# Kernel tuning notes

Measured on AMD Instinct MI355X. Metric: run time of the kernel, lower is better.

## Reference

```python
import jax, jax.numpy as jnp
import numpy as np

B, D, C = 4096, 1024, 11003
SCALE = 28.0
EPS_LS = 0.1
T = 4.0
L2, L3, L4 = 1.0, 1.0, 1.0
ALPHA, BETA = 0.6, 0.4
SPOS, SNEG = 10.0, 40.0
HDR_ALPHA, HDR_BETA, PLEN = 3.0, 3.0, 63


def setup_inputs() -> dict:
    key = jax.random.key(0)
    k1, k2, k3, k4, k5 = jax.random.split(key, 5)
    return {
        "visual_embed": jax.random.normal(k1, (B, D), dtype=jnp.float32),
        "textual_embed": jax.random.normal(k2, (B, D), dtype=jnp.float32),
        "labels": jax.random.randint(k3, (B,), 0, C, dtype=jnp.int64)
        if jax.config.read("jax_enable_x64") else jax.random.randint(k3, (B,), 0, C, dtype=jnp.int32),
        "W": jax.random.normal(k4, (D, C), dtype=jnp.float32) * (6.0 / (D + C)) ** 0.5,
        "W_text": jax.random.normal(k5, (D, C), dtype=jnp.float32) * (6.0 / (D + C)) ** 0.5,
    }


def _l2norm(x, axis):
    return x / jnp.linalg.norm(x, axis=axis, keepdims=True)


def _label_smooth_ce(logits, labels):
    # CrossEntropyLabelSmooth with epsilon=0.1
    lp = jax.nn.log_softmax(logits, axis=1)
    n, c = logits.shape
    picked = jnp.take_along_axis(lp, labels[:, None], axis=1)[:, 0]
    return -((1.0 - EPS_LS) * picked + (EPS_LS / c) * lp.sum(axis=1)).mean()


def _pdist(e, eps=1e-12):
    sq = (e * e).sum(axis=1)
    d2 = jnp.maximum(sq[:, None] + sq[None, :] - 2.0 * (e @ e.T), eps)
    d = jnp.sqrt(d2)
    return d * (1.0 - jnp.eye(e.shape[0], dtype=d.dtype))  # zero diagonal


def _hard_dark_rank(student, teacher):
    score_t = -HDR_ALPHA * _pdist(teacher) ** HDR_BETA
    score_s = -HDR_ALPHA * _pdist(student) ** HDR_BETA
    # top PLEN neighbors of teacher (skip self at rank 0), descending sort
    permute_idx = jnp.argsort(-score_t, axis=1)[:, 1 : PLEN + 1]  # [B, PLEN]
    ordered = jnp.take_along_axis(score_s, permute_idx, axis=1)  # [B, PLEN]
    # logsumexp over suffixes ordered[:, i:] == reversed cumulative logsumexp
    rev = jnp.flip(ordered, axis=1)
    lse_tail = jnp.flip(jax.lax.cumlogsumexp(rev, axis=1), axis=1)
    log_prob = (ordered - lse_tail).sum(axis=1)
    return (-log_prob).mean()


def _kl_div(student_logits, teacher_logits):
    s = jax.nn.softmax(student_logits / T, axis=1)
    t = jax.nn.softmax(jax.lax.stop_gradient(teacher_logits) / T, axis=1)
    log_s = jnp.log(jnp.maximum(s, 1e-12))
    log_t = jnp.log(jnp.maximum(t, 1e-12))
    return (((log_t - log_s) * t).sum(axis=1)).mean()


def reference(visual_embed, textual_embed, labels, W, W_text):
    vn = _l2norm(visual_embed, axis=1)
    tn = _l2norm(textual_embed, axis=1)
    Wn = W / jnp.linalg.norm(W, axis=0, keepdims=True)
    Wtn = W_text / jnp.linalg.norm(W_text, axis=0, keepdims=True)

    visual_logits = SCALE * (vn @ Wn)   # [B, C]
    textual_logits = SCALE * (tn @ Wn)  # [B, C]

    v_loss = _label_smooth_ce(visual_logits, labels)
    t_loss = _label_smooth_ce(textual_logits, labels)

    # distillation (LAMBDA2 feature L2 + LAMBDA3 KL on logits)
    vf = jax.lax.stop_gradient(vn)
    dist_f = ((vf - tn) ** 2).sum(axis=1).mean()
    dist_p = _kl_div(textual_logits, visual_logits)
    distillation = L2 * dist_f + L3 * dist_p

    # W_text filter CE (LAMBDA4 branch)
    t_filter = L4 * _label_smooth_ce(SCALE * (tn @ Wtn), labels)

    # HardDarkRank (Flickr30K branch): student=textual, teacher=detached visual
    loss_hdr = _hard_dark_rank(tn, jax.lax.stop_gradient(vn))

    instance = v_loss + t_loss + t_filter + distillation + 0.1 * loss_hdr

    # global_align_loss, fully vectorized. The original loops over rows AND
    # columns so every (i,j) pair is counted twice.
    sim = vn @ tn.T  # [B, B]
    mask = labels[:, None] == labels[None, :]
    loss_pos = jnp.log1p(jnp.exp(-SPOS * (sim - ALPHA)))
    loss_neg = jnp.log1p(jnp.exp(SNEG * (sim - BETA)))
    global_align = 2.0 * jnp.where(mask, loss_pos, loss_neg).sum() / sim.shape[0]

    return instance + global_align
```

## Files before the change

kernel.cpp:

```cpp
#include <hip/hip_runtime.h>
#include <math.h>

#define Bn 4096
#define Dn 1024
#define Cn 11003
#define Cpad 11008
#define NCTL 86
#define NQ 9
#define NT 32
#define NTRI 528

typedef __attribute__((ext_vector_type(8))) short bf16x8;
typedef __attribute__((ext_vector_type(4))) float f32x4;

__device__ __forceinline__ unsigned short f2bf(float f) {
  union { float f; unsigned u; } v; v.f = f;
  unsigned r = (v.u + 0x7fffu + ((v.u >> 16) & 1u)) >> 16;
  return (unsigned short)r;
}
__device__ __forceinline__ float bf2f(unsigned short h) {
  union { unsigned u; float f; } v; v.u = ((unsigned)h) << 16;
  return v.f;
}

__device__ __forceinline__ void stage16(const unsigned short* g, unsigned short* l) {
  __builtin_amdgcn_global_load_lds(
      (const __attribute__((address_space(1))) void*)g,
      (__attribute__((address_space(3))) void*)l, 16, 0, 0);
}

#define SRC_BLK(tid) (((tid) & 7) ^ (((tid) >> 3) & 7))
#define FRAG(buf, R, KB) (*(const bf16x8*)((buf) + (R) * 64 + (((KB) ^ ((R) & 7)) * 8)))

__device__ __forceinline__ float blk_sum256(float v, volatile float* sb) {
#pragma unroll
  for (int o = 32; o > 0; o >>= 1) v += __shfl_down(v, o, 64);
  __syncthreads();
  if ((threadIdx.x & 63) == 0) sb[threadIdx.x >> 6] = v;
  __syncthreads();
  return sb[0] + sb[1] + sb[2] + sb[3];
}

__global__ void zero_acc_k(float* acc) {
  if (threadIdx.x < 8) acc[threadIdx.x] = 0.f;
}

__global__ __launch_bounds__(256) void rownorm_k(const float* __restrict__ x,
                                                 unsigned short* __restrict__ yh,
                                                 float* __restrict__ sq) {
  __shared__ float sb[4];
  int r = blockIdx.x;
  const float* xr = x + (size_t)r * Dn;
  float s = 0.f;
  for (int k = threadIdx.x; k < Dn; k += 256) { float v = xr[k]; s += v * v; }
  s = blk_sum256(s, sb);
  float nrm = sqrtf(s);
  float s2 = 0.f;
  for (int k = threadIdx.x; k < Dn; k += 256) {
    float v = xr[k] / nrm;
    yh[(size_t)r * Dn + k] = f2bf(v);
    s2 += v * v;
  }
  s2 = blk_sum256(s2, sb);
  if (threadIdx.x == 0) sq[r] = s2;
}

__global__ __launch_bounds__(256) void colnorm_k(const float* __restrict__ W,
                                                 float* __restrict__ rn) {
  int c = blockIdx.x * 256 + threadIdx.x;
  if (c >= Cn) return;
  float s = 0.f;
  for (int d = 0; d < Dn; ++d) { float v = W[(size_t)d * Cn + c]; s += v * v; }
  rn[c] = 1.f / sqrtf(s);
}

__global__ __launch_bounds__(256) void transpose_k(const float* __restrict__ W,
                                                   const float* __restrict__ rn,
                                                   unsigned short* __restrict__ WT) {
  __shared__ float T[64][65];
  const int c0 = blockIdx.x * 64, d0 = blockIdx.y * 64;
  const int tid = threadIdx.x;
  const int cl = tid & 63;
  for (int dl = tid >> 6; dl < 64; dl += 4) {
    float v = (c0 + cl < Cn) ? W[(size_t)(d0 + dl) * Cn + c0 + cl] : 0.f;
    T[cl][dl] = v;
  }
  __syncthreads();
  const int dd = tid & 63;
  for (int co = tid >> 6; co < 64; co += 4) {
    int c = c0 + co;
    unsigned short o = 0;
    if (c < Cn) o = f2bf(T[co][dd] * rn[c]);
    WT[(size_t)c * Dn + d0 + dd] = o;
  }
}

__global__ __launch_bounds__(256, 2) void logits_vt_k(
    const unsigned short* __restrict__ vnh, const unsigned short* __restrict__ tnh,
    const unsigned short* __restrict__ WnT, float* __restrict__ part) {
  __shared__ __align__(16) unsigned short Av[128 * 64];
  __shared__ __align__(16) unsigned short At[128 * 64];
  __shared__ __align__(16) unsigned short Bs[128 * 64];
  __shared__ float qsum[7 * 128];

  const int rt = blockIdx.x, ct = blockIdx.y;
  const int r0 = rt * 128, c0 = ct * 128;
  const int tid = threadIdx.x;
  const int lane = tid & 63;
  const int wid = tid >> 6;
  const int wr = (wid >> 1) * 64, wc = (wid & 1) * 64;
  const int m = lane & 15, q = lane >> 4;

  for (int t = tid; t < 7 * 128; t += 256) qsum[t] = 0.f;

  const f32x4 zero4 = {0.f, 0.f, 0.f, 0.f};
  f32x4 accV[4][4], accT[4][4];
#pragma unroll
  for (int i = 0; i < 4; ++i)
#pragma unroll
    for (int j = 0; j < 4; ++j) { accV[i][j] = zero4; accT[i][j] = zero4; }

  const int srow = tid >> 3;
  const int skc = SRC_BLK(tid) * 8;

  for (int kk = 0; kk < 16; ++kk) {
    const int k0 = kk * 64;
#pragma unroll
    for (int p = 0; p < 4; ++p) {
      stage16(vnh + (size_t)(r0 + p * 32 + srow) * Dn + k0 + skc, Av + p * 2048 + tid * 8);
      stage16(tnh + (size_t)(r0 + p * 32 + srow) * Dn + k0 + skc, At + p * 2048 + tid * 8);
      stage16(WnT + (size_t)(c0 + p * 32 + srow) * Dn + k0 + skc, Bs + p * 2048 + tid * 8);
    }
    __syncthreads();
#pragma unroll
    for (int ks = 0; ks < 2; ++ks) {
      const int KB = ks * 4 + q;
      bf16x8 av[4], at[4], bb[4];
#pragma unroll
      for (int f = 0; f < 4; ++f) {
        av[f] = FRAG(Av, wr + f * 16 + m, KB);
        at[f] = FRAG(At, wr + f * 16 + m, KB);
        bb[f] = FRAG(Bs, wc + f * 16 + m, KB);
      }
#pragma unroll
      for (int i = 0; i < 4; ++i)
#pragma unroll
        for (int j = 0; j < 4; ++j) {
          accV[i][j] = __builtin_amdgcn_mfma_f32_16x16x32_bf16(av[i], bb[j], accV[i][j], 0, 0, 0);
          accT[i][j] = __builtin_amdgcn_mfma_f32_16x16x32_bf16(at[i], bb[j], accT[i][j], 0, 0, 0);
        }
    }
    __syncthreads();
  }

#pragma unroll
  for (int i = 0; i < 4; ++i) {
#pragma unroll
    for (int r = 0; r < 4; ++r) {
      const int rowl = wr + i * 16 + q * 4 + r;
      float s0 = 0.f, s1 = 0.f, s2 = 0.f, s3 = 0.f, s6 = 0.f, s7 = 0.f, s8 = 0.f;
#pragma unroll
      for (int j = 0; j < 4; ++j) {
        int col = c0 + wc + j * 16 + m;
        if (col < Cn) {
          float V = 28.f * accV[i][j][r];
          float T = 28.f * accT[i][j][r];
          float ev4 = __expf((V - 28.f) * 0.25f);
          float et4 = __expf((T - 28.f) * 0.25f);
          float ev2 = ev4 * ev4, et2 = et4 * et4;
          s0 += ev2 * ev2;
          s1 += V;
          s2 += et2 * et2;
          s3 += T;
          s6 += ev4;
          s7 += et4;
          s8 += ev4 * (V - T);
        }
      }
#pragma unroll
      for (int o = 1; o < 16; o <<= 1) {
        s0 += __shfl_xor(s0, o, 64); s1 += __shfl_xor(s1, o, 64);
        s2 += __shfl_xor(s2, o, 64); s3 += __shfl_xor(s3, o, 64);
        s6 += __shfl_xor(s6, o, 64); s7 += __shfl_xor(s7, o, 64);
        s8 += __shfl_xor(s8, o, 64);
      }
      if (m == 0) {
        atomicAdd(&qsum[0 * 128 + rowl], s0);
        atomicAdd(&qsum[1 * 128 + rowl], s1);
        atomicAdd(&qsum[2 * 128 + rowl], s2);
        atomicAdd(&qsum[3 * 128 + rowl], s3);
        atomicAdd(&qsum[4 * 128 + rowl], s6);
        atomicAdd(&qsum[5 * 128 + rowl], s7);
        atomicAdd(&qsum[6 * 128 + rowl], s8);
      }
    }
  }
  __syncthreads();
  if (tid < 128) {
    size_t base = (size_t)ct * Bn + r0 + tid;
    const size_t qs = (size_t)NCTL * Bn;
    part[0 * qs + base] = qsum[0 * 128 + tid];
    part[1 * qs + base] = qsum[1 * 128 + tid];
    part[2 * qs + base] = qsum[2 * 128 + tid];
    part[3 * qs + base] = qsum[3 * 128 + tid];
    part[6 * qs + base] = qsum[4 * 128 + tid];
    part[7 * qs + base] = qsum[5 * 128 + tid];
    part[8 * qs + base] = qsum[6 * 128 + tid];
  }
}

__global__ __launch_bounds__(256, 2) void logits_f_k(
    const unsigned short* __restrict__ tnh, const unsigned short* __restrict__ WtnT,
    float* __restrict__ part) {
  __shared__ __align__(16) unsigned short Aa[256 * 64];
  __shared__ __align__(16) unsigned short Bs[128 * 64];
  __shared__ float qsum[2 * 256];

  const int rt = blockIdx.x, ct = blockIdx.y;
  const int r0 = rt * 256, c0 = ct * 128;
  const int tid = threadIdx.x;
  const int lane = tid & 63;
  const int wid = tid >> 6;
  const int wr = (wid >> 1) * 128, wc = (wid & 1) * 64;
  const int m = lane & 15, q = lane >> 4;

  for (int t = tid; t < 2 * 256; t += 256) qsum[t] = 0.f;

  const f32x4 zero4 = {0.f, 0.f, 0.f, 0.f};
  f32x4 acc[8][4];
#pragma unroll
  for (int i = 0; i < 8; ++i)
#pragma unroll
    for (int j = 0; j < 4; ++j) acc[i][j] = zero4;

  const int srow = tid >> 3;
  const int skc = SRC_BLK(tid) * 8;

  for (int kk = 0; kk < 16; ++kk) {
    const int k0 = kk * 64;
#pragma unroll
    for (int p = 0; p < 8; ++p)
      stage16(tnh + (size_t)(r0 + p * 32 + srow) * Dn + k0 + skc, Aa + p * 2048 + tid * 8);
#pragma unroll
    for (int p = 0; p < 4; ++p)
      stage16(WtnT + (size_t)(c0 + p * 32 + srow) * Dn + k0 + skc, Bs + p * 2048 + tid * 8);
    __syncthreads();
#pragma unroll
    for (int ks = 0; ks < 2; ++ks) {
      const int KB = ks * 4 + q;
      bf16x8 aa[8], bb[4];
#pragma unroll
      for (int f = 0; f < 8; ++f) aa[f] = FRAG(Aa, wr + f * 16 + m, KB);
#pragma unroll
      for (int f = 0; f < 4; ++f) bb[f] = FRAG(Bs, wc + f * 16 + m, KB);
#pragma unroll
      for (int i = 0; i < 8; ++i)
#pragma unroll
        for (int j = 0; j < 4; ++j)
          acc[i][j] = __builtin_amdgcn_mfma_f32_16x16x32_bf16(aa[i], bb[j], acc[i][j], 0, 0, 0);
    }
    __syncthreads();
  }

#pragma unroll
  for (int i = 0; i < 8; ++i) {
#pragma unroll
    for (int r = 0; r < 4; ++r) {
      const int rowl = wr + i * 16 + q * 4 + r;
      float s4 = 0.f, s5 = 0.f;
#pragma unroll
      for (int j = 0; j < 4; ++j) {
        int col = c0 + wc + j * 16 + m;
        if (col < Cn) {
          float F = 28.f * acc[i][j][r];
          s4 += __expf(F - 28.f);
          s5 += F;
        }
      }
#pragma unroll
      for (int o = 1; o < 16; o <<= 1) {
        s4 += __shfl_xor(s4, o, 64);
        s5 += __shfl_xor(s5, o, 64);
      }
      if (m == 0) {
        atomicAdd(&qsum[0 * 256 + rowl], s4);
        atomicAdd(&qsum[1 * 256 + rowl], s5);
      }
    }
  }
  __syncthreads();
  {
    size_t base = (size_t)ct * Bn + r0 + tid;
    const size_t qs = (size_t)NCTL * Bn;
    part[4 * qs + base] = qsum[0 * 256 + tid];
    part[5 * qs + base] = qsum[1 * 256 + tid];
  }
}

__global__ __launch_bounds__(256, 3) void gramsym_f32_k(const unsigned short* __restrict__ A,
                                                        float* __restrict__ G) {
  __shared__ __align__(16) unsigned short Aa[128 * 64];
  __shared__ __align__(16) unsigned short Bs[128 * 64];
  int t = blockIdx.x, it = 0, rem = NT;
  while (t >= rem) { t -= rem; ++it; --rem; }
  const int jt = it + t;
  const int i0 = it * 128, j0 = jt * 128;
  const int tid = threadIdx.x;
  const int lane = tid & 63;
  const int wid = tid >> 6;
  const int wr = (wid >> 1) * 64, wc = (wid & 1) * 64;
  const int m = lane & 15, q = lane >> 4;

  const f32x4 zero4 = {0.f, 0.f, 0.f, 0.f};
  f32x4 acc[4][4];
#pragma unroll
  for (int i = 0; i < 4; ++i)
#pragma unroll
    for (int j = 0; j < 4; ++j) acc[i][j] = zero4;

  const int srow = tid >> 3;
  const int skc = SRC_BLK(tid) * 8;

  for (int kk = 0; kk < 16; ++kk) {
    const int k0 = kk * 64;
#pragma unroll
    for (int p = 0; p < 4; ++p) {
      stage16(A + (size_t)(i0 + p * 32 + srow) * Dn + k0 + skc, Aa + p * 2048 + tid * 8);
      stage16(A + (size_t)(j0 + p * 32 + srow) * Dn + k0 + skc, Bs + p * 2048 + tid * 8);
    }
    __syncthreads();
#pragma unroll
    for (int ks = 0; ks < 2; ++ks) {
      const int KB = ks * 4 + q;
      bf16x8 aa[4], bb[4];
#pragma unroll
      for (int f = 0; f < 4; ++f) {
        aa[f] = FRAG(Aa, wr + f * 16 + m, KB);
        bb[f] = FRAG(Bs, wc + f * 16 + m, KB);
      }
#pragma unroll
      for (int i = 0; i < 4; ++i)
#pragma unroll
        for (int j = 0; j < 4; ++j)
          acc[i][j] = __builtin_amdgcn_mfma_f32_16x16x32_bf16(aa[i], bb[j], acc[i][j], 0, 0, 0);
    }
    __syncthreads();
  }
#pragma unroll
  for (int i = 0; i < 4; ++i)
#pragma unroll
    for (int j = 0; j < 4; ++j)
#pragma unroll
      for (int r = 0; r < 4; ++r) {
        int row = wr + i * 16 + q * 4 + r, col = wc + j * 16 + m;
        G[(size_t)(i0 + row) * Bn + j0 + col] = acc[i][j][r];
        if (it != jt) G[(size_t)(j0 + col) * Bn + i0 + row] = acc[i][j][r];
      }
}

__global__ __launch_bounds__(256, 3) void gramsym_bf16_k(const unsigned short* __restrict__ A,
                                                         unsigned short* __restrict__ G) {
  __shared__ __align__(16) unsigned short Aa[128 * 64];
  __shared__ __align__(16) unsigned short Bs[128 * 64];
  int t = blockIdx.x, it = 0, rem = NT;
  while (t >= rem) { t -= rem; ++it; --rem; }
  const int jt = it + t;
  const int i0 = it * 128, j0 = jt * 128;
  const int tid = threadIdx.x;
  const int lane = tid & 63;
  const int wid = tid >> 6;
  const int wr = (wid >> 1) * 64, wc = (wid & 1) * 64;
  const int m = lane & 15, q = lane >> 4;

  const f32x4 zero4 = {0.f, 0.f, 0.f, 0.f};
  f32x4 acc[4][4];
#pragma unroll
  for (int i = 0; i < 4; ++i)
#pragma unroll
    for (int j = 0; j < 4; ++j) acc[i][j] = zero4;

  const int srow = tid >> 3;
  const int skc = SRC_BLK(tid) * 8;

  for (int kk = 0; kk < 16; ++kk) {
    const int k0 = kk * 64;
#pragma unroll
    for (int p = 0; p < 4; ++p) {
      stage16(A + (size_t)(i0 + p * 32 + srow) * Dn + k0 + skc, Aa + p * 2048 + tid * 8);
      stage16(A + (size_t)(j0 + p * 32 + srow) * Dn + k0 + skc, Bs + p * 2048 + tid * 8);
    }
    __syncthreads();
#pragma unroll
    for (int ks = 0; ks < 2; ++ks) {
      const int KB = ks * 4 + q;
      bf16x8 aa[4], bb[4];
#pragma unroll
      for (int f = 0; f < 4; ++f) {
        aa[f] = FRAG(Aa, wr + f * 16 + m, KB);
        bb[f] = FRAG(Bs, wc + f * 16 + m, KB);
      }
#pragma unroll
      for (int i = 0; i < 4; ++i)
#pragma unroll
        for (int j = 0; j < 4; ++j)
          acc[i][j] = __builtin_amdgcn_mfma_f32_16x16x32_bf16(aa[i], bb[j], acc[i][j], 0, 0, 0);
    }
    __syncthreads();
  }
#pragma unroll
  for (int i = 0; i < 4; ++i)
#pragma unroll
    for (int j = 0; j < 4; ++j)
#pragma unroll
      for (int r = 0; r < 4; ++r) {
        int row = wr + i * 16 + q * 4 + r, col = wc + j * 16 + m;
        unsigned short h = f2bf(acc[i][j][r]);
        G[(size_t)(i0 + row) * Bn + j0 + col] = h;
        if (it != jt) G[(size_t)(j0 + col) * Bn + i0 + row] = h;
      }
}

__global__ __launch_bounds__(256, 3) void align_k(const unsigned short* __restrict__ vnh,
                                                  const unsigned short* __restrict__ tnh,
                                                  const int* __restrict__ labels,
                                                  float* __restrict__ accbuf) {
  __shared__ __align__(16) unsigned short Aa[128 * 64];
  __shared__ __align__(16) unsigned short Bs[128 * 64];
  __shared__ int li_s[128], lj_s[128];
  __shared__ float sb[4];
  const int jt = blockIdx.x, it = blockIdx.y;
  const int j0 = jt * 128, i0 = it * 128;
  const int tid = threadIdx.x;
  const int lane = tid & 63;
  const int wid = tid >> 6;
  const int wr = (wid >> 1) * 64, wc = (wid & 1) * 64;
  const int m = lane & 15, q = lane >> 4;

  if (tid < 128) li_s[tid] = labels[i0 + tid];
  else lj_s[tid - 128] = labels[j0 + tid - 128];

  const f32x4 zero4 = {0.f, 0.f, 0.f, 0.f};
  f32x4 acc[4][4];
#pragma unroll
  for (int i = 0; i < 4; ++i)
#pragma unroll
    for (int j = 0; j < 4; ++j) acc[i][j] = zero4;

  const int srow = tid >> 3;
  const int skc = SRC_BLK(tid) * 8;

  for (int kk = 0; kk < 16; ++kk) {
    const int k0 = kk * 64;
#pragma unroll
    for (int p = 0; p < 4; ++p) {
      stage16(vnh + (size_t)(i0 + p * 32 + srow) * Dn + k0 + skc, Aa + p * 2048 + tid * 8);
      stage16(tnh + (size_t)(j0 + p * 32 + srow) * Dn + k0 + skc, Bs + p * 2048 + tid * 8);
    }
    __syncthreads();
#pragma unroll
    for (int ks = 0; ks < 2; ++ks) {
      const int KB = ks * 4 + q;
      bf16x8 aa[4], bb[4];
#pragma unroll
      for (int f = 0; f < 4; ++f) {
        aa[f] = FRAG(Aa, wr + f * 16 + m, KB);
        bb[f] = FRAG(Bs, wc + f * 16 + m, KB);
      }
#pragma unroll
      for (int i = 0; i < 4; ++i)
#pragma unroll
        for (int j = 0; j < 4; ++j)
          acc[i][j] = __builtin_amdgcn_mfma_f32_16x16x32_bf16(aa[i], bb[j], acc[i][j], 0, 0, 0);
    }
    __syncthreads();
  }

  float ls = 0.f;
#pragma unroll
  for (int i = 0; i < 4; ++i)
#pragma unroll
    for (int r = 0; r < 4; ++r) {
      int li = li_s[wr + i * 16 + q * 4 + r];
#pragma unroll
      for (int j = 0; j < 4; ++j) {
        int lj = lj_s[wc + j * 16 + m];
        float s = acc[i][j][r];
        float x = (li == lj) ? (-10.f * (s - 0.6f)) : (40.f * (s - 0.4f));
        ls += fmaxf(x, 0.f) + __logf(1.f + __expf(-fabsf(x)));
      }
    }
  float tot = blk_sum256(ls, sb);
  if (tid == 0) atomicAdd(&accbuf[1], tot);
}

__global__ __launch_bounds__(256) void picked_k(const unsigned short* __restrict__ vnh,
                                                const unsigned short* __restrict__ tnh,
                                                const unsigned short* __restrict__ WnT,
                                                const unsigned short* __restrict__ WtnT,
                                                const int* __restrict__ labels,
                                                float* __restrict__ pv, float* __restrict__ pt,
                                                float* __restrict__ pf, float* __restrict__ df) {
  __shared__ float sb[4];
  int r = blockIdx.x;
  int lab = labels[r];
  float spv = 0.f, spt = 0.f, spf = 0.f, sdf = 0.f;
  for (int k = threadIdx.x; k < Dn; k += 256) {
    float a = bf2f(vnh[(size_t)r * Dn + k]);
    float b = bf2f(tnh[(size_t)r * Dn + k]);
    float w = bf2f(WnT[(size_t)lab * Dn + k]);
    float wt = bf2f(WtnT[(size_t)lab * Dn + k]);
    spv += a * w;
    spt += b * w;
    spf += b * wt;
    float dd = a - b;
    sdf += dd * dd;
  }
  spv = blk_sum256(spv, sb);
  spt = blk_sum256(spt, sb);
  spf = blk_sum256(spf, sb);
  sdf = blk_sum256(sdf, sb);
  if (threadIdx.x == 0) {
    pv[r] = 28.f * spv;
    pt[r] = 28.f * spt;
    pf[r] = 28.f * spf;
    df[r] = sdf;
  }
}

__global__ __launch_bounds__(256) void finalize_k(const float* __restrict__ part,
                                                  const float* __restrict__ pv,
                                                  const float* __restrict__ pt,
                                                  const float* __restrict__ pf,
                                                  const float* __restrict__ df,
                                                  float* __restrict__ accbuf) {
  __shared__ float sb[4];
  int r = blockIdx.x * 256 + threadIdx.x;
  float s[NQ];
#pragma unroll
  for (int q = 0; q < NQ; ++q) s[q] = 0.f;
  const size_t qs = (size_t)NCTL * Bn;
  for (int ct = 0; ct < NCTL; ++ct) {
#pragma unroll
    for (int q = 0; q < NQ; ++q) s[q] += part[(size_t)q * qs + (size_t)ct * Bn + r];
  }
  float lseV = logf(s[0]) + 28.f;
  float lseT = logf(s[2]) + 28.f;
  float lseF = logf(s[4]) + 28.f;
  const float invC = 1.f / (float)Cn;
  float ceV = -(0.9f * (pv[r] - lseV) + 0.1f * invC * (s[1] - (float)Cn * lseV));
  float ceT = -(0.9f * (pt[r] - lseT) + 0.1f * invC * (s[3] - (float)Cn * lseT));
  float ceF = -(0.9f * (pf[r] - lseF) + 0.1f * invC * (s[5] - (float)Cn * lseF));
  float kl = s[8] / (4.f * s[6]) + logf(s[7]) - logf(s[6]);
  float row = ceV + ceT + ceF + kl + df[r];
  float tot = blk_sum256(row, sb);
  if (threadIdx.x == 0) atomicAdd(&accbuf[0], tot / (float)Bn);
}

__device__ __forceinline__ int kswz(int j) {
  return (j & ~63) | ((j ^ (j >> 6)) & 63);
}
__device__ __forceinline__ unsigned long long shflx_u64(unsigned long long v, int o) {
  int lo = __shfl_xor((int)(unsigned)v, o, 64);
  int hi = __shfl_xor((int)(unsigned)(v >> 32), o, 64);
  return ((unsigned long long)(unsigned)hi << 32) | (unsigned)lo;
}

__global__ __launch_bounds__(256) void hdr_k(const float* __restrict__ Gv,
                                             const unsigned short* __restrict__ Gtb,
                                             const float* __restrict__ sqv,
                                             const float* __restrict__ sqt,
                                             float* __restrict__ accbuf) {
  __shared__ float key[Bn];
  __shared__ int selIdx[64];
  __shared__ float selS[64];
  const int i = blockIdx.x, tid = threadIdx.x;
  const int lane = tid & 63, wid = tid >> 6;
  const float INF = __builtin_inff();
  float sqi = sqv[i];
  const float4* gv4 = (const float4*)(Gv + (size_t)i * Bn);
  const float4* sq4 = (const float4*)sqv;
  for (int j4 = tid; j4 < Bn / 4; j4 += 256) {
    float4 g = gv4[j4];
    float4 s = sq4[j4];
    int j = j4 * 4;
    key[kswz(j + 0)] = (j + 0 == i) ? INF : fmaxf(sqi + s.x - 2.f * g.x, 1e-12f);
    key[kswz(j + 1)] = (j + 1 == i) ? INF : fmaxf(sqi + s.y - 2.f * g.y, 1e-12f);
    key[kswz(j + 2)] = (j + 2 == i) ? INF : fmaxf(sqi + s.z - 2.f * g.z, 1e-12f);
    key[kswz(j + 3)] = (j + 3 == i) ? INF : fmaxf(sqi + s.w - 2.f * g.w, 1e-12f);
  }
  __syncthreads();

  if (wid == 0) {
    unsigned long long best = ~0ull;
    for (int k = 0; k < 64; ++k) {
      int j = k * 64 + lane;
      float v = key[kswz(j)];
      unsigned long long p = ((unsigned long long)__float_as_uint(v) << 32) | (unsigned)j;
      if (p < best) best = p;
    }
    for (int it = 0; it < 63; ++it) {
      unsigned long long w = best;
#pragma unroll
      for (int o = 32; o > 0; o >>= 1) {
        unsigned long long ow = shflx_u64(w, o);
        if (ow < w) w = ow;
      }
      int bj = (int)(unsigned)w;
      if (lane == 0) selIdx[it] = bj;
      int s = bj & 63;
      int kj = (lane << 6) | s;
      int sidx = kswz(kj);
      float kv = key[sidx];
      if (kj == bj) { kv = INF; key[sidx] = INF; }
      unsigned long long p = ((unsigned long long)__float_as_uint(kv) << 32) | (unsigned)kj;
#pragma unroll
      for (int o = 32; o > 0; o >>= 1) {
        unsigned long long op = shflx_u64(p, o);
        if (op < p) p = op;
      }
      if (lane == s) best = p;
    }
  }
  __syncthreads();

  if (tid < 63) {
    int j = selIdx[tid];
    float g = bf2f(Gtb[(size_t)i * Bn + j]);
    float d2 = fmaxf(sqt[i] + sqt[j] - 2.f * g, 1e-12f);
    selS[tid] = -3.f * sqrtf(d2) * d2;
  }
  __syncthreads();

  if (tid == 0) {
    float lse = selS[62];
    float loss = 0.f;
    for (int k = 61; k >= 0; --k) {
      float a = fmaxf(lse, selS[k]);
      lse = a + logf(__expf(lse - a) + __expf(selS[k] - a));
      loss += lse - selS[k];
    }
    atomicAdd(&accbuf[2], loss);
  }
}

__global__ void combine_k(const float* __restrict__ accbuf, float* __restrict__ out) {
  out[0] = accbuf[0] + (2.f / (float)Bn) * accbuf[1] + (0.1f / (float)Bn) * accbuf[2];
}

extern "C" void kernel_launch(void* const* d_in, const int* in_sizes, int n_in,
                              void* d_out, int out_size, void* d_ws, size_t ws_size,
                              hipStream_t stream) {
  const float* ve = (const float*)d_in[0];
  const float* te = (const float*)d_in[1];
  const int* labels = (const int*)d_in[2];
  const float* W = (const float*)d_in[3];
  const float* Wt = (const float*)d_in[4];
  float* out = (float*)d_out;

  char* base = (char*)d_ws;
  size_t off = 0;
  unsigned short* vnh = (unsigned short*)(base + off);  off += (size_t)Bn * Dn * 2;
  unsigned short* tnh = (unsigned short*)(base + off);  off += (size_t)Bn * Dn * 2;
  unsigned short* WnT = (unsigned short*)(base + off);  off += (size_t)Cpad * Dn * 2;
  unsigned short* WtnT = (unsigned short*)(base + off); off += (size_t)Cpad * Dn * 2;
  float* Gv = (float*)(base + off);          off += (size_t)Bn * Bn * 4;
  unsigned short* Gtb = (unsigned short*)(base + off); off += (size_t)Bn * Bn * 2;
  float* part = (float*)(base + off);        off += (size_t)NQ * NCTL * Bn * 4;
  float* rnW = (float*)(base + off);         off += (size_t)Cpad * 4;
  float* rnWt = (float*)(base + off);        off += (size_t)Cpad * 4;
  float* sqv = (float*)(base + off);         off += (size_t)Bn * 4;
  float* sqt = (float*)(base + off);         off += (size_t)Bn * 4;
  float* pv = (float*)(base + off);          off += (size_t)Bn * 4;
  float* pt = (float*)(base + off);          off += (size_t)Bn * 4;
  float* pf = (float*)(base + off);          off += (size_t)Bn * 4;
  float* df = (float*)(base + off);          off += (size_t)Bn * 4;
  float* acc = (float*)(base + off);         off += 64;

  zero_acc_k<<<1, 64, 0, stream>>>(acc);
  rownorm_k<<<Bn, 256, 0, stream>>>(ve, vnh, sqv);
  rownorm_k<<<Bn, 256, 0, stream>>>(te, tnh, sqt);
  colnorm_k<<<(Cn + 255) / 256, 256, 0, stream>>>(W, rnW);
  colnorm_k<<<(Cn + 255) / 256, 256, 0, stream>>>(Wt, rnWt);
  transpose_k<<<dim3(Cpad / 64, Dn / 64), 256, 0, stream>>>(W, rnW, WnT);
  transpose_k<<<dim3(Cpad / 64, Dn / 64), 256, 0, stream>>>(Wt, rnWt, WtnT);
  logits_vt_k<<<dim3(Bn / 128, NCTL), 256, 0, stream>>>(vnh, tnh, WnT, part);
  logits_f_k<<<dim3(Bn / 256, NCTL), 256, 0, stream>>>(tnh, WtnT, part);
  gramsym_f32_k<<<NTRI, 256, 0, stream>>>(vnh, Gv);
  gramsym_bf16_k<<<NTRI, 256, 0, stream>>>(tnh, Gtb);
  align_k<<<dim3(Bn / 128, Bn / 128), 256, 0, stream>>>(vnh, tnh, labels, acc);
  picked_k<<<Bn, 256, 0, stream>>>(vnh, tnh, WnT, WtnT, labels, pv, pt, pf, df);
  finalize_k<<<Bn / 256, 256, 0, stream>>>(part, pv, pt, pf, df, acc);
  hdr_k<<<Bn, 256, 0, stream>>>(Gv, Gtb, sqv, sqt, acc);
  combine_k<<<1, 1, 0, stream>>>(acc, out);
}
```

Baseline: 979.0 us.

## Switch logits GEMMs to 32x32 MFMA, fuse gram with align, merge launches

The logits kernels now use the 32x32x16 bf16 MFMA instruction instead of 16x16x32, which means fewer LDS fragment reads per FLOP, and the row reductions are reworked to match the new accumulator layout. The symmetric f32 visual gram kernel and the align kernel are fused into one full-grid kernel. It shares the visual A tile, computes both G and the align loss, and writes G without using symmetry. The paired norm, colnorm and transpose launches are each merged into a single launch through a grid dimension. The fused kernel gives up the triangular saving on the visual gram, trading extra MFMA work for one fewer pass over the inputs.

```diff
diff --git a/kernel.cpp b/kernel.cpp
--- a/kernel.cpp
+++ b/kernel.cpp
@@ -12,6 +12,7 @@
 
 typedef __attribute__((ext_vector_type(8))) short bf16x8;
 typedef __attribute__((ext_vector_type(4))) float f32x4;
+typedef __attribute__((ext_vector_type(16))) float f32x16;
 
 __device__ __forceinline__ unsigned short f2bf(float f) {
   union { float f; unsigned u; } v; v.f = f;
@@ -45,10 +46,16 @@
   if (threadIdx.x < 8) acc[threadIdx.x] = 0.f;
 }
 
-__global__ __launch_bounds__(256) void rownorm_k(const float* __restrict__ x,
-                                                 unsigned short* __restrict__ yh,
-                                                 float* __restrict__ sq) {
+__global__ __launch_bounds__(256) void rownorm_k(const float* __restrict__ xv,
+                                                 const float* __restrict__ xt,
+                                                 unsigned short* __restrict__ yv,
+                                                 unsigned short* __restrict__ yt,
+                                                 float* __restrict__ sqv,
+                                                 float* __restrict__ sqt) {
   __shared__ float sb[4];
+  const float* x = blockIdx.y ? xt : xv;
+  unsigned short* y = blockIdx.y ? yt : yv;
+  float* sq = blockIdx.y ? sqt : sqv;
   int r = blockIdx.x;
   const float* xr = x + (size_t)r * Dn;
   float s = 0.f;
@@ -58,7 +65,7 @@
   float s2 = 0.f;
   for (int k = threadIdx.x; k < Dn; k += 256) {
     float v = xr[k] / nrm;
-    yh[(size_t)r * Dn + k] = f2bf(v);
+    y[(size_t)r * Dn + k] = f2bf(v);
     s2 += v * v;
   }
   s2 = blk_sum256(s2, sb);
@@ -66,23 +73,33 @@
 }
 
 __global__ __launch_bounds__(256) void colnorm_k(const float* __restrict__ W,
-                                                 float* __restrict__ rn) {
+                                                 const float* __restrict__ Wt,
+                                                 float* __restrict__ rnW,
+                                                 float* __restrict__ rnWt) {
+  const float* X = blockIdx.y ? Wt : W;
+  float* rn = blockIdx.y ? rnWt : rnW;
   int c = blockIdx.x * 256 + threadIdx.x;
   if (c >= Cn) return;
   float s = 0.f;
-  for (int d = 0; d < Dn; ++d) { float v = W[(size_t)d * Cn + c]; s += v * v; }
+  for (int d = 0; d < Dn; ++d) { float v = X[(size_t)d * Cn + c]; s += v * v; }
   rn[c] = 1.f / sqrtf(s);
 }
 
 __global__ __launch_bounds__(256) void transpose_k(const float* __restrict__ W,
-                                                   const float* __restrict__ rn,
-                                                   unsigned short* __restrict__ WT) {
+                                                   const float* __restrict__ Wt,
+                                                   const float* __restrict__ rnW,
+                                                   const float* __restrict__ rnWt,
+                                                   unsigned short* __restrict__ WnT,
+                                                   unsigned short* __restrict__ WtnT) {
   __shared__ float T[64][65];
+  const float* X = blockIdx.z ? Wt : W;
+  const float* rn = blockIdx.z ? rnWt : rnW;
+  unsigned short* WT = blockIdx.z ? WtnT : WnT;
   const int c0 = blockIdx.x * 64, d0 = blockIdx.y * 64;
   const int tid = threadIdx.x;
   const int cl = tid & 63;
   for (int dl = tid >> 6; dl < 64; dl += 4) {
-    float v = (c0 + cl < Cn) ? W[(size_t)(d0 + dl) * Cn + c0 + cl] : 0.f;
+    float v = (c0 + cl < Cn) ? X[(size_t)(d0 + dl) * Cn + c0 + cl] : 0.f;
     T[cl][dl] = v;
   }
   __syncthreads();
@@ -109,16 +126,17 @@
   const int lane = tid & 63;
   const int wid = tid >> 6;
   const int wr = (wid >> 1) * 64, wc = (wid & 1) * 64;
-  const int m = lane & 15, q = lane >> 4;
+  const int l31 = lane & 31, half = lane >> 5;
 
   for (int t = tid; t < 7 * 128; t += 256) qsum[t] = 0.f;
 
-  const f32x4 zero4 = {0.f, 0.f, 0.f, 0.f};
-  f32x4 accV[4][4], accT[4][4];
-#pragma unroll
-  for (int i = 0; i < 4; ++i)
-#pragma unroll
-    for (int j = 0; j < 4; ++j) { accV[i][j] = zero4; accT[i][j] = zero4; }
+  f32x16 accV[2][2], accT[2][2];
+#pragma unroll
+  for (int i = 0; i < 2; ++i)
+#pragma unroll
+    for (int j = 0; j < 2; ++j)
+#pragma unroll
+      for (int e = 0; e < 16; ++e) { accV[i][j][e] = 0.f; accT[i][j][e] = 0.f; }
 
   const int srow = tid >> 3;
   const int skc = SRC_BLK(tid) * 8;
@@ -133,38 +151,38 @@
     }
     __syncthreads();
 #pragma unroll
-    for (int ks = 0; ks < 2; ++ks) {
-      const int KB = ks * 4 + q;
-      bf16x8 av[4], at[4], bb[4];
-#pragma unroll
-      for (int f = 0; f < 4; ++f) {
-        av[f] = FRAG(Av, wr + f * 16 + m, KB);
-        at[f] = FRAG(At, wr + f * 16 + m, KB);
-        bb[f] = FRAG(Bs, wc + f * 16 + m, KB);
-      }
-#pragma unroll
-      for (int i = 0; i < 4; ++i)
-#pragma unroll
-        for (int j = 0; j < 4; ++j) {
-          accV[i][j] = __builtin_amdgcn_mfma_f32_16x16x32_bf16(av[i], bb[j], accV[i][j], 0, 0, 0);
-          accT[i][j] = __builtin_amdgcn_mfma_f32_16x16x32_bf16(at[i], bb[j], accT[i][j], 0, 0, 0);
+    for (int t = 0; t < 4; ++t) {
+      const int KB = t * 2 + half;
+      bf16x8 av[2], at[2], bb[2];
+#pragma unroll
+      for (int f = 0; f < 2; ++f) {
+        av[f] = FRAG(Av, wr + f * 32 + l31, KB);
+        at[f] = FRAG(At, wr + f * 32 + l31, KB);
+        bb[f] = FRAG(Bs, wc + f * 32 + l31, KB);
+      }
+#pragma unroll
+      for (int i = 0; i < 2; ++i)
+#pragma unroll
+        for (int j = 0; j < 2; ++j) {
+          accV[i][j] = __builtin_amdgcn_mfma_f32_32x32x16_bf16(av[i], bb[j], accV[i][j], 0, 0, 0);
+          accT[i][j] = __builtin_amdgcn_mfma_f32_32x32x16_bf16(at[i], bb[j], accT[i][j], 0, 0, 0);
         }
     }
     __syncthreads();
   }
 
 #pragma unroll
-  for (int i = 0; i < 4; ++i) {
-#pragma unroll
-    for (int r = 0; r < 4; ++r) {
-      const int rowl = wr + i * 16 + q * 4 + r;
+  for (int bi = 0; bi < 2; ++bi) {
+#pragma unroll
+    for (int r = 0; r < 16; ++r) {
+      const int rowl = wr + bi * 32 + (r & 3) + 8 * (r >> 2) + 4 * half;
       float s0 = 0.f, s1 = 0.f, s2 = 0.f, s3 = 0.f, s6 = 0.f, s7 = 0.f, s8 = 0.f;
 #pragma unroll
-      for (int j = 0; j < 4; ++j) {
-        int col = c0 + wc + j * 16 + m;
+      for (int bj = 0; bj < 2; ++bj) {
+        int col = c0 + wc + bj * 32 + l31;
         if (col < Cn) {
-          float V = 28.f * accV[i][j][r];
-          float T = 28.f * accT[i][j][r];
+          float V = 28.f * accV[bi][bj][r];
+          float T = 28.f * accT[bi][bj][r];
           float ev4 = __expf((V - 28.f) * 0.25f);
           float et4 = __expf((T - 28.f) * 0.25f);
           float ev2 = ev4 * ev4, et2 = et4 * et4;
@@ -178,13 +196,13 @@
         }
       }
 #pragma unroll
-      for (int o = 1; o < 16; o <<= 1) {
+      for (int o = 1; o < 32; o <<= 1) {
         s0 += __shfl_xor(s0, o, 64); s1 += __shfl_xor(s1, o, 64);
         s2 += __shfl_xor(s2, o, 64); s3 += __shfl_xor(s3, o, 64);
         s6 += __shfl_xor(s6, o, 64); s7 += __shfl_xor(s7, o, 64);
         s8 += __shfl_xor(s8, o, 64);
       }
-      if (m == 0) {
+      if (l31 == 0) {
         atomicAdd(&qsum[0 * 128 + rowl], s0);
         atomicAdd(&qsum[1 * 128 + rowl], s1);
         atomicAdd(&qsum[2 * 128 + rowl], s2);
@@ -222,16 +240,17 @@
   const int lane = tid & 63;
   const int wid = tid >> 6;
   const int wr = (wid >> 1) * 128, wc = (wid & 1) * 64;
-  const int m = lane & 15, q = lane >> 4;
+  const int l31 = lane & 31, half = lane >> 5;
 
   for (int t = tid; t < 2 * 256; t += 256) qsum[t] = 0.f;
 
-  const f32x4 zero4 = {0.f, 0.f, 0.f, 0.f};
-  f32x4 acc[8][4];
-#pragma unroll
-  for (int i = 0; i < 8; ++i)
-#pragma unroll
-    for (int j = 0; j < 4; ++j) acc[i][j] = zero4;
+  f32x16 acc[4][2];
+#pragma unroll
+  for (int i = 0; i < 4; ++i)
+#pragma unroll
+    for (int j = 0; j < 2; ++j)
+#pragma unroll
+      for (int e = 0; e < 16; ++e) acc[i][j][e] = 0.f;
 
   const int srow = tid >> 3;
   const int skc = SRC_BLK(tid) * 8;
@@ -246,43 +265,43 @@
       stage16(WtnT + (size_t)(c0 + p * 32 + srow) * Dn + k0 + skc, Bs + p * 2048 + tid * 8);
     __syncthreads();
 #pragma unroll
-    for (int ks = 0; ks < 2; ++ks) {
-      const int KB = ks * 4 + q;
-      bf16x8 aa[8], bb[4];
-#pragma unroll
-      for (int f = 0; f < 8; ++f) aa[f] = FRAG(Aa, wr + f * 16 + m, KB);
-#pragma unroll
-      for (int f = 0; f < 4; ++f) bb[f] = FRAG(Bs, wc + f * 16 + m, KB);
-#pragma unroll
-      for (int i = 0; i < 8; ++i)
-#pragma unroll
-        for (int j = 0; j < 4; ++j)
-          acc[i][j] = __builtin_amdgcn_mfma_f32_16x16x32_bf16(aa[i], bb[j], acc[i][j], 0, 0, 0);
-    }
-    __syncthreads();
-  }
-
-#pragma unroll
-  for (int i = 0; i < 8; ++i) {
-#pragma unroll
-    for (int r = 0; r < 4; ++r) {
-      const int rowl = wr + i * 16 + q * 4 + r;
+    for (int t = 0; t < 4; ++t) {
+      const int KB = t * 2 + half;
+      bf16x8 aa[4], bb[2];
+#pragma unroll
+      for (int f = 0; f < 4; ++f) aa[f] = FRAG(Aa, wr + f * 32 + l31, KB);
+#pragma unroll
+      for (int f = 0; f < 2; ++f) bb[f] = FRAG(Bs, wc + f * 32 + l31, KB);
+#pragma unroll
+      for (int i = 0; i < 4; ++i)
+#pragma unroll
+        for (int j = 0; j < 2; ++j)
+          acc[i][j] = __builtin_amdgcn_mfma_f32_32x32x16_bf16(aa[i], bb[j], acc[i][j], 0, 0, 0);
+    }
+    __syncthreads();
+  }
+
+#pragma unroll
+  for (int bi = 0; bi < 4; ++bi) {
+#pragma unroll
+    for (int r = 0; r < 16; ++r) {
+      const int rowl = wr + bi * 32 + (r & 3) + 8 * (r >> 2) + 4 * half;
       float s4 = 0.f, s5 = 0.f;
 #pragma unroll
-      for (int j = 0; j < 4; ++j) {
-        int col = c0 + wc + j * 16 + m;
+      for (int bj = 0; bj < 2; ++bj) {
+        int col = c0 + wc + bj * 32 + l31;
         if (col < Cn) {
-          float F = 28.f * acc[i][j][r];
+          float F = 28.f * acc[bi][bj][r];
           s4 += __expf(F - 28.f);
           s5 += F;
         }
       }
 #pragma unroll
-      for (int o = 1; o < 16; o <<= 1) {
+      for (int o = 1; o < 32; o <<= 1) {
         s4 += __shfl_xor(s4, o, 64);
         s5 += __shfl_xor(s5, o, 64);
       }
-      if (m == 0) {
+      if (l31 == 0) {
         atomicAdd(&qsum[0 * 256 + rowl], s4);
         atomicAdd(&qsum[1 * 256 + rowl], s5);
       }
@@ -297,26 +316,31 @@
   }
 }
 
-__global__ __launch_bounds__(256, 3) void gramsym_f32_k(const unsigned short* __restrict__ A,
-                                                        float* __restrict__ G) {
+__global__ __launch_bounds__(256, 2) void gramv_align_k(
+    const unsigned short* __restrict__ vnh, const unsigned short* __restrict__ tnh,
+    const int* __restrict__ labels, float* __restrict__ G, float* __restrict__ accbuf) {
   __shared__ __align__(16) unsigned short Aa[128 * 64];
-  __shared__ __align__(16) unsigned short Bs[128 * 64];
-  int t = blockIdx.x, it = 0, rem = NT;
-  while (t >= rem) { t -= rem; ++it; --rem; }
-  const int jt = it + t;
-  const int i0 = it * 128, j0 = jt * 128;
+  __shared__ __align__(16) unsigned short Vb[128 * 64];
+  __shared__ __align__(16) unsigned short Tb[128 * 64];
+  __shared__ int li_s[128], lj_s[128];
+  __shared__ float sb[4];
+  const int jt = blockIdx.x, it = blockIdx.y;
+  const int j0 = jt * 128, i0 = it * 128;
   const int tid = threadIdx.x;
   const int lane = tid & 63;
   const int wid = tid >> 6;
   const int wr = (wid >> 1) * 64, wc = (wid & 1) * 64;
   const int m = lane & 15, q = lane >> 4;
 
+  if (tid < 128) li_s[tid] = labels[i0 + tid];
+  else lj_s[tid - 128] = labels[j0 + tid - 128];
+
   const f32x4 zero4 = {0.f, 0.f, 0.f, 0.f};
-  f32x4 acc[4][4];
+  f32x4 accG[4][4], accS[4][4];
 #pragma unroll
   for (int i = 0; i < 4; ++i)
 #pragma unroll
-    for (int j = 0; j < 4; ++j) acc[i][j] = zero4;
+    for (int j = 0; j < 4; ++j) { accG[i][j] = zero4; accS[i][j] = zero4; }
 
   const int srow = tid >> 3;
   const int skc = SRC_BLK(tid) * 8;
@@ -325,37 +349,51 @@
     const int k0 = kk * 64;
 #pragma unroll
     for (int p = 0; p < 4; ++p) {
-      stage16(A + (size_t)(i0 + p * 32 + srow) * Dn + k0 + skc, Aa + p * 2048 + tid * 8);
-      stage16(A + (size_t)(j0 + p * 32 + srow) * Dn + k0 + skc, Bs + p * 2048 + tid * 8);
+      stage16(vnh + (size_t)(i0 + p * 32 + srow) * Dn + k0 + skc, Aa + p * 2048 + tid * 8);
+      stage16(vnh + (size_t)(j0 + p * 32 + srow) * Dn + k0 + skc, Vb + p * 2048 + tid * 8);
+      stage16(tnh + (size_t)(j0 + p * 32 + srow) * Dn + k0 + skc, Tb + p * 2048 + tid * 8);
     }
     __syncthreads();
 #pragma unroll
     for (int ks = 0; ks < 2; ++ks) {
       const int KB = ks * 4 + q;
-      bf16x8 aa[4], bb[4];
+      bf16x8 aa[4], vb[4], tb[4];
 #pragma unroll
       for (int f = 0; f < 4; ++f) {
         aa[f] = FRAG(Aa, wr + f * 16 + m, KB);
-        bb[f] = FRAG(Bs, wc + f * 16 + m, KB);
+        vb[f] = FRAG(Vb, wc + f * 16 + m, KB);
+        tb[f] = FRAG(Tb, wc + f * 16 + m, KB);
       }
 #pragma unroll
       for (int i = 0; i < 4; ++i)
 #pragma unroll
-        for (int j = 0; j < 4; ++j)
-          acc[i][j] = __builtin_amdgcn_mfma_f32_16x16x32_bf16(aa[i], bb[j], acc[i][j], 0, 0, 0);
-    }
-    __syncthreads();
-  }
+        for (int j = 0; j < 4; ++j) {
+          accG[i][j] = __builtin_amdgcn_mfma_f32_16x16x32_bf16(aa[i], vb[j], accG[i][j], 0, 0, 0);
+          accS[i][j] = __builtin_amdgcn_mfma_f32_16x16x32_bf16(aa[i], tb[j], accS[i][j], 0, 0, 0);
+        }
+    }
+    __syncthreads();
+  }
+
+  float ls = 0.f;
 #pragma unroll
   for (int i = 0; i < 4; ++i)
 #pragma unroll
-    for (int j = 0; j < 4; ++j)
-#pragma unroll
-      for (int r = 0; r < 4; ++r) {
-        int row = wr + i * 16 + q * 4 + r, col = wc + j * 16 + m;
-        G[(size_t)(i0 + row) * Bn + j0 + col] = acc[i][j][r];
-        if (it != jt) G[(size_t)(j0 + col) * Bn + i0 + row] = acc[i][j][r];
-      }
+    for (int r = 0; r < 4; ++r) {
+      int rowl = wr + i * 16 + q * 4 + r;
+      int li = li_s[rowl];
+#pragma unroll
+      for (int j = 0; j < 4; ++j) {
+        int coll = wc + j * 16 + m;
+        G[(size_t)(i0 + rowl) * Bn + j0 + coll] = accG[i][j][r];
+        int lj = lj_s[coll];
+        float s = accS[i][j][r];
+        float x = (li == lj) ? (-10.f * (s - 0.6f)) : (40.f * (s - 0.4f));
+        ls += fmaxf(x, 0.f) + __logf(1.f + __expf(-fabsf(x)));
+      }
+    }
+  float tot = blk_sum256(ls, sb);
+  if (tid == 0) atomicAdd(&accbuf[1], tot);
 }
 
 __global__ __launch_bounds__(256, 3) void gramsym_bf16_k(const unsigned short* __restrict__ A,
@@ -418,79 +456,6 @@
         G[(size_t)(i0 + row) * Bn + j0 + col] = h;
         if (it != jt) G[(size_t)(j0 + col) * Bn + i0 + row] = h;
       }
-}
-
-__global__ __launch_bounds__(256, 3) void align_k(const unsigned short* __restrict__ vnh,
-                                                  const unsigned short* __restrict__ tnh,
-                                                  const int* __restrict__ labels,
-                                                  float* __restrict__ accbuf) {
-  __shared__ __align__(16) unsigned short Aa[128 * 64];
-  __shared__ __align__(16) unsigned short Bs[128 * 64];
-  __shared__ int li_s[128], lj_s[128];
-  __shared__ float sb[4];
-  const int jt = blockIdx.x, it = blockIdx.y;
-  const int j0 = jt * 128, i0 = it * 128;
-  const int tid = threadIdx.x;
-  const int lane = tid & 63;
-  const int wid = tid >> 6;
-  const int wr = (wid >> 1) * 64, wc = (wid & 1) * 64;
-  const int m = lane & 15, q = lane >> 4;
-
-  if (tid < 128) li_s[tid] = labels[i0 + tid];
-  else lj_s[tid - 128] = labels[j0 + tid - 128];
-
-  const f32x4 zero4 = {0.f, 0.f, 0.f, 0.f};
-  f32x4 acc[4][4];
-#pragma unroll
-  for (int i = 0; i < 4; ++i)
-#pragma unroll
-    for (int j = 0; j < 4; ++j) acc[i][j] = zero4;
-
-  const int srow = tid >> 3;
-  const int skc = SRC_BLK(tid) * 8;
-
-  for (int kk = 0; kk < 16; ++kk) {
-    const int k0 = kk * 64;
-#pragma unroll
-    for (int p = 0; p < 4; ++p) {
-      stage16(vnh + (size_t)(i0 + p * 32 + srow) * Dn + k0 + skc, Aa + p * 2048 + tid * 8);
-      stage16(tnh + (size_t)(j0 + p * 32 + srow) * Dn + k0 + skc, Bs + p * 2048 + tid * 8);
-    }
-    __syncthreads();
-#pragma unroll
-    for (int ks = 0; ks < 2; ++ks) {
-      const int KB = ks * 4 + q;
-      bf16x8 aa[4], bb[4];
-#pragma unroll
-      for (int f = 0; f < 4; ++f) {
-        aa[f] = FRAG(Aa, wr + f * 16 + m, KB);
-        bb[f] = FRAG(Bs, wc + f * 16 + m, KB);
-      }
-#pragma unroll
-      for (int i = 0; i < 4; ++i)
-#pragma unroll
-        for (int j = 0; j < 4; ++j)
-          acc[i][j] = __builtin_amdgcn_mfma_f32_16x16x32_bf16(aa[i], bb[j], acc[i][j], 0, 0, 0);
-    }
-    __syncthreads();
-  }
-
-  float ls = 0.f;
-#pragma unroll
-  for (int i = 0; i < 4; ++i)
-#pragma unroll
-    for (int r = 0; r < 4; ++r) {
-      int li = li_s[wr + i * 16 + q * 4 + r];
-#pragma unroll
-      for (int j = 0; j < 4; ++j) {
-        int lj = lj_s[wc + j * 16 + m];
-        float s = acc[i][j][r];
-        float x = (li == lj) ? (-10.f * (s - 0.6f)) : (40.f * (s - 0.4f));
-        ls += fmaxf(x, 0.f) + __logf(1.f + __expf(-fabsf(x)));
-      }
-    }
-  float tot = blk_sum256(ls, sb);
-  if (tid == 0) atomicAdd(&accbuf[1], tot);
 }
 
 __global__ __launch_bounds__(256) void picked_k(const unsigned short* __restrict__ vnh,
@@ -677,17 +642,13 @@
   float* acc = (float*)(base + off);         off += 64;
 
   zero_acc_k<<<1, 64, 0, stream>>>(acc);
-  rownorm_k<<<Bn, 256, 0, stream>>>(ve, vnh, sqv);
-  rownorm_k<<<Bn, 256, 0, stream>>>(te, tnh, sqt);
-  colnorm_k<<<(Cn + 255) / 256, 256, 0, stream>>>(W, rnW);
-  colnorm_k<<<(Cn + 255) / 256, 256, 0, stream>>>(Wt, rnWt);
-  transpose_k<<<dim3(Cpad / 64, Dn / 64), 256, 0, stream>>>(W, rnW, WnT);
-  transpose_k<<<dim3(Cpad / 64, Dn / 64), 256, 0, stream>>>(Wt, rnWt, WtnT);
+  rownorm_k<<<dim3(Bn, 2), 256, 0, stream>>>(ve, te, vnh, tnh, sqv, sqt);
+  colnorm_k<<<dim3((Cn + 255) / 256, 2), 256, 0, stream>>>(W, Wt, rnW, rnWt);
+  transpose_k<<<dim3(Cpad / 64, Dn / 64, 2), 256, 0, stream>>>(W, Wt, rnW, rnWt, WnT, WtnT);
   logits_vt_k<<<dim3(Bn / 128, NCTL), 256, 0, stream>>>(vnh, tnh, WnT, part);
   logits_f_k<<<dim3(Bn / 256, NCTL), 256, 0, stream>>>(tnh, WtnT, part);
-  gramsym_f32_k<<<NTRI, 256, 0, stream>>>(vnh, Gv);
+  gramv_align_k<<<dim3(NT, NT), 256, 0, stream>>>(vnh, tnh, labels, Gv, acc);
   gramsym_bf16_k<<<NTRI, 256, 0, stream>>>(tnh, Gtb);
-  align_k<<<dim3(Bn / 128, Bn / 128), 256, 0, stream>>>(vnh, tnh, labels, acc);
   picked_k<<<Bn, 256, 0, stream>>>(vnh, tnh, WnT, WtnT, labels, pv, pt, pf, df);
   finalize_k<<<Bn / 256, 256, 0, stream>>>(part, pv, pt, pf, df, acc);
   hdr_k<<<Bn, 256, 0, stream>>>(Gv, Gtb, sqv, sqt, acc);
```

Result: slower. 1.026 ms (+4.8%).
